# Optimization experiments

Hardware: AMD Instinct MI355X
Metric: run time of the kernel (lower is better)

The kernel has to match this reference:

```python
import jax, jax.numpy as jnp
import numpy as np

NSAMPLE = 1024
KNN = [16, 32, 64]
MLP = [[32, 32, 64], [64, 64, 128], [64, 96, 128]]
IN_CH = 3
EPS = 1e-5  # torch BatchNorm2d default eps


def fps(points, nsample):
    """Farthest point sampling. Deterministic start at index 0 (torch version uses a
    random start index; the algorithm/math is otherwise identical)."""
    B, N, _ = points.shape
    xyz = points[..., :3]

    def body(i, st):
        dist, far, idx = st
        idx = idx.at[:, i].set(far)
        c = jnp.take_along_axis(xyz, far[:, None, None], axis=1)  # [B,1,3]
        d = jnp.sum((xyz - c) ** 2, axis=-1)                      # [B,N]
        dist = jnp.minimum(dist, d)
        far = jnp.argmax(dist, axis=1).astype(jnp.int32)
        return dist, far, idx

    dist0 = jnp.full((B, N), 1e10, points.dtype)
    far0 = jnp.zeros((B,), jnp.int32)
    idx0 = jnp.zeros((B, nsample), jnp.int32)
    _, _, idx = jax.lax.fori_loop(0, nsample, body, (dist0, far0, idx0))
    return jnp.take_along_axis(points, idx[..., None], axis=1)  # [B,nsample,C]


def knn_idx(points, query, k):
    # Squared euclidean distances preserve the knn ordering of torch.cdist(p=2).
    q = query[..., :3]
    p = points[..., :3]
    d2 = (jnp.sum(q * q, -1)[:, :, None]
          - 2.0 * jnp.einsum('bqc,bnc->bqn', q, p)
          + jnp.sum(p * p, -1)[:, None, :])          # [B,S,N]
    return jax.lax.top_k(-d2, k)[1]                  # [B,S,k] smallest-k indices


def gather_groups(points, idx):
    return jax.vmap(lambda p, ix: p[ix])(points, idx)  # [B,S,k,C]


def mlp_branch(x, params):
    # x: [B,S,K,Cin]; 1x1 Conv2d == per-point linear; BN in training mode (batch stats).
    for w, b, g, be in params:
        x = jnp.einsum('bskc,oc->bsko', x, w) + b
        m = jnp.mean(x, axis=(0, 1, 2))
        v = jnp.var(x, axis=(0, 1, 2))
        x = jax.nn.relu((x - m) * jax.lax.rsqrt(v + EPS) * g + be)
    return jnp.max(x, axis=2)  # max-pool over neighbors -> [B,S,Cout]


def setup_inputs() -> dict:
    key = jax.random.key(0)
    ks = jax.random.split(key, 16)
    inp = {"points": jax.random.normal(ks[0], (8, 8192, 3), jnp.float32)}
    t = 1
    for i, block in enumerate(MLP):
        last = IN_CH
        for j, out in enumerate(block):
            inp[f"w{i}{j}"] = 0.1 * jax.random.normal(ks[t % 16], (out, last), jnp.float32)
            inp[f"b{i}{j}"] = jnp.zeros((out,), jnp.float32)
            inp[f"g{i}{j}"] = jnp.ones((out,), jnp.float32)
            inp[f"be{i}{j}"] = jnp.zeros((out,), jnp.float32)
            last = out
            t += 1
    return inp


def reference(points,
              w00, b00, g00, be00, w01, b01, g01, be01, w02, b02, g02, be02,
              w10, b10, g10, be10, w11, b11, g11, be11, w12, b12, g12, be12,
              w20, b20, g20, be20, w21, b21, g21, be21, w22, b22, g22, be22):
    params = [
        [(w00, b00, g00, be00), (w01, b01, g01, be01), (w02, b02, g02, be02)],
        [(w10, b10, g10, be10), (w11, b11, g11, be11), (w12, b12, g12, be12)],
        [(w20, b20, g20, be20), (w21, b21, g21, be21), (w22, b22, g22, be22)],
    ]
    # FPS is deterministic here, so the per-branch recomputation in the torch code
    # yields identical centroids; compute once.
    centroids = fps(points, NSAMPLE)
    feats = []
    for i, k in enumerate(KNN):
        idx = knn_idx(points, centroids, k)
        grouped = gather_groups(points, idx)
        feats.append(mlp_branch(grouped, params[i]))
    return jnp.concatenate(feats, axis=-1)  # [B, nsample, 320]
```

## Files before the change

kernel.cpp:

```cpp
#include <hip/hip_runtime.h>
#include <hip/hip_fp16.h>

#define DEVFN __device__ __forceinline__

typedef _Float16 v2h __attribute__((ext_vector_type(2)));

DEVFN float fdot2(v2h a, v2h b, float c) {
#if __has_builtin(__builtin_amdgcn_fdot2)
  return __builtin_amdgcn_fdot2(a, b, c, false);
#else
  return c + (float)a[0] * (float)b[0] + (float)a[1] * (float)b[1];
#endif
}

struct OpSum { DEVFN float operator()(float a, float b) const { return a + b; } };

template<int CH, int D, typename OP, int NV>
DEVFN void halve(float (&v)[NV], int lane, int& base) {
  if constexpr (D >= 1) {
    OP op;
    if constexpr (CH > 1) {
      constexpr int H = CH / 2;
      #pragma unroll
      for (int i = 0; i < H; ++i) {
        float send = (lane & D) ? v[i] : v[H + i];
        float r = __shfl_xor(send, D);
        float keep = (lane & D) ? v[H + i] : v[i];
        v[i] = op(keep, r);
      }
      if (lane & D) base += H;
      halve<H, (D >> 1), OP, NV>(v, lane, base);
    } else {
      v[0] = op(v[0], __shfl_xor(v[0], D));
      halve<CH, (D >> 1), OP, NV>(v, lane, base);
    }
  }
}

template<int CC, int NA, int T>
DEVFN void do_stats_w(const float (&a)[NA], float m, int tid, float* spart,
                      float* prow, int statoff) {
  float v[2 * CC];
  #pragma unroll
  for (int j = 0; j < CC; ++j) { float x = a[j]; v[2 * j] = m * x; v[2 * j + 1] = m * x * x; }
  int lane = tid & 63, base = 0;
  halve<2 * CC, 32, OpSum, 2 * CC>(v, lane, base);
  int wv = tid >> 6;
  spart[wv * 256 + base] = v[0];
  __syncthreads();
  constexpr int NW = T / 64;
  if (tid < 2 * CC) {
    float s2 = 0.f;
    #pragma unroll
    for (int w = 0; w < NW; ++w) s2 += spart[w * 256 + tid];
    prow[statoff + tid] = s2;
  }
  __syncthreads();
}

__global__ __launch_bounds__(512) void fps_kernel(const float* __restrict__ pts,
                                                  float4* __restrict__ cent) {
  const int b = blockIdx.x, t = threadIdx.x;
  const int wv = t >> 6;
  __shared__ unsigned long long sk2[2][8];
  __shared__ float4 sc4[2][8];
  __shared__ float4 scent[1024];
  const float* p = pts + (size_t)b * 8192 * 3;
  float px[16], py[16], pz[16], dd[16];
  #pragma unroll
  for (int j = 0; j < 16; ++j) {
    const int i = t + j * 512;
    px[j] = p[i * 3]; py[j] = p[i * 3 + 1]; pz[j] = p[i * 3 + 2];
    dd[j] = 1e10f;
  }
  float cx = p[0], cy = p[1], cz = p[2];
  for (int it = 0; it < 1024; ++it) {
    if (t == 0) scent[it] = make_float4(cx, cy, cz, 0.f);
    const int par = it & 1;
    float bd = -1.f, bx = 0.f, by = 0.f, bz = 0.f; int bi = 0;
    #pragma unroll
    for (int j = 0; j < 16; ++j) {
      const float dx = px[j] - cx, dy = py[j] - cy, dz = pz[j] - cz;
      float d = fminf(dd[j], dx * dx + dy * dy + dz * dz);
      dd[j] = d;
      if (d > bd) { bd = d; bi = t + j * 512; bx = px[j]; by = py[j]; bz = pz[j]; }
    }
    float wmax = bd;
    #pragma unroll
    for (int m = 32; m >= 1; m >>= 1) wmax = fmaxf(wmax, __shfl_xor(wmax, m));
    const unsigned long long am = __ballot(bd == wmax);
    bool iswin;
    if (__popcll(am) == 1) {
      iswin = (bd == wmax);
    } else {
      int cand = (bd == wmax) ? bi : 0x7FFFFFFF;
      #pragma unroll
      for (int m = 32; m >= 1; m >>= 1) cand = min(cand, __shfl_xor(cand, m));
      iswin = (bd == wmax) && (bi == cand);
    }
    if (iswin) {
      sk2[par][wv] = ((unsigned long long)__float_as_uint(bd) << 32)
                     | (0xFFFFFFFFu - (unsigned)bi);
      sc4[par][wv] = make_float4(bx, by, bz, 0.f);
    }
    __syncthreads();
    unsigned long long gk = sk2[par][0];
    float4 c4 = sc4[par][0];
    #pragma unroll
    for (int w = 1; w < 8; ++w) {
      const unsigned long long k2 = sk2[par][w];
      const float4 cc = sc4[par][w];
      if (k2 > gk) { gk = k2; c4 = cc; }
    }
    cx = c4.x; cy = c4.y; cz = c4.z;
  }
  __syncthreads();
  #pragma unroll
  for (int i = t; i < 1024; i += 512) cent[(size_t)b * 1024 + i] = scent[i];
}

__global__ __launch_bounds__(256) void knn_kernel(const float* __restrict__ pts,
                                                  const float4* __restrict__ cent,
                                                  int* __restrict__ knn) {
  const int wid = (blockIdx.x * 256 + threadIdx.x) >> 6;
  const int lane = threadIdx.x & 63;
  const int b = wid >> 10;
  const float4 q = cent[wid];
  const float q2 = q.x * q.x + q.y * q.y + q.z * q.z;
  const float* p = pts + (size_t)b * 8192 * 3;
  unsigned long long R = ~0ull;
  for (int c0 = 0; c0 < 8192; c0 += 64) {
    const int i = c0 + lane;
    const float x = p[i * 3], y = p[i * 3 + 1], z = p[i * 3 + 2];
    const float p2 = x * x + y * y + z * z;
    const float dot = q.x * x + q.y * y + q.z * z;
    float d2 = q2 - 2.f * dot + p2;
    d2 = fmaxf(d2, 0.f);
    unsigned u = __float_as_uint(d2);
    u = (u & 0x80000000u) ? ~u : (u | 0x80000000u);
    const unsigned long long key = ((unsigned long long)u << 32) | (unsigned)i;
    const unsigned long long rmax = __shfl(R, 63);
    unsigned long long mask = __ballot(key < rmax);
    while (mask) {
      const int src = __ffsll(mask) - 1;
      mask &= mask - 1;
      const unsigned long long nk = __shfl(key, src);
      const int pos = __popcll(__ballot(R < nk));
      if (pos < 64) {
        const unsigned long long Rm1 = __shfl_up(R, 1);
        R = (lane < pos) ? R : (lane == pos ? nk : Rm1);
      }
    }
  }
  knn[wid * 64 + lane] = (int)(R & 0xffffffffu);
}

__global__ __launch_bounds__(256) void moments_kernel(const float* __restrict__ pts,
                                                      const int* __restrict__ knn_,
                                                      float* __restrict__ mpart) {
  __shared__ float smom[4][27];
  const int tid = threadIdx.x, lane = tid & 63, wv = tid >> 6;
  const int samp = blockIdx.x * 4 + wv;
  const int b = samp >> 10;
  const int pidx = knn_[samp * 64 + lane];
  const float* pp = pts + ((size_t)b * 8192 + pidx) * 3;
  const float x = pp[0], y = pp[1], z = pp[2];
  float g[9] = {x, y, z, x * x, x * y, x * z, y * y, y * z, z * z};
  #pragma unroll
  for (int m = 8; m >= 1; m >>= 1) {
    #pragma unroll
    for (int i = 0; i < 9; ++i) g[i] += __shfl_xor(g[i], m);
  }
  float h[9], tot[9];
  #pragma unroll
  for (int i = 0; i < 9; ++i) h[i] = g[i] + __shfl_xor(g[i], 16);
  #pragma unroll
  for (int i = 0; i < 9; ++i) tot[i] = h[i] + __shfl_xor(h[i], 32);
  if (lane == 0) {
    #pragma unroll
    for (int i = 0; i < 9; ++i) {
      smom[wv][i] = g[i]; smom[wv][9 + i] = h[i]; smom[wv][18 + i] = tot[i];
    }
  }
  __syncthreads();
  if (tid < 27) {
    mpart[blockIdx.x * 32 + tid] =
        smom[0][tid] + smom[1][tid] + smom[2][tid] + smom[3][tid];
  }
}

__global__ __launch_bounds__(256) void finalize0_kernel(const float* __restrict__ mpart,
    const float* __restrict__ w00, const float* __restrict__ b00,
    const float* __restrict__ g00, const float* __restrict__ be00,
    const float* __restrict__ w01, const float* __restrict__ b01,
    const float* __restrict__ g01, const float* __restrict__ be01,
    const float* __restrict__ w02, const float* __restrict__ b02,
    const float* __restrict__ g02, const float* __restrict__ be02,
    float* __restrict__ scsh) {
  __shared__ float fsum[8][32];
  __shared__ float mom[32];
  const int t = threadIdx.x;
  const int col = t & 31, chunk = t >> 5;
  float s = 0.f;
  for (int r = chunk * 256; r < chunk * 256 + 256; ++r) s += mpart[r * 32 + col];
  fsum[chunk][col] = s;
  __syncthreads();
  if (t < 32) {
    float s2 = 0.f;
    #pragma unroll
    for (int c = 0; c < 8; ++c) s2 += fsum[c][t];
    mom[t] = s2;
  }
  __syncthreads();
  int o; const float *w, *bb, *gg, *be; float E; int base, br;
  if (t < 32)       { br = 0; o = t;      w = w00; bb = b00; gg = g00; be = be00; E = 131072.f; base = 0; }
  else if (t < 96)  { br = 1; o = t - 32; w = w01; bb = b01; gg = g01; be = be01; E = 262144.f; base = 9; }
  else if (t < 160) { br = 2; o = t - 96; w = w02; bb = b02; gg = g02; be = be02; E = 524288.f; base = 18; }
  else return;
  const float Sx = mom[base], Sy = mom[base + 1], Sz = mom[base + 2];
  const float mxx = mom[base + 3], mxy = mom[base + 4], mxz = mom[base + 5];
  const float myy = mom[base + 6], myz = mom[base + 7], mzz = mom[base + 8];
  const float W0 = w[o * 3], W1 = w[o * 3 + 1], W2 = w[o * 3 + 2], bo = bb[o];
  const float wS = W0 * Sx + W1 * Sy + W2 * Sz;
  const float qf = W0 * W0 * mxx + 2.f * W0 * W1 * mxy + 2.f * W0 * W2 * mxz
                 + W1 * W1 * myy + 2.f * W1 * W2 * myz + W2 * W2 * mzz;
  const float mean = wS / E + bo;
  const float msq = (qf + 2.f * bo * wS) / E + bo * bo;
  const float var = msq - mean * mean;
  const float inv = 1.0f / sqrtf(var + 1e-5f);
  const float sc = gg[o] * inv;
  scsh[br * 768 + o] = sc;
  scsh[br * 768 + 128 + o] = be[o] - mean * sc;
}

__global__ __launch_bounds__(256) void pack_kernel(
    const float* __restrict__ w1a, const float* __restrict__ w1b, const float* __restrict__ w1c,
    const float* __restrict__ w2a, const float* __restrict__ w2b, const float* __restrict__ w2c,
    v2h* __restrict__ w1h2, v2h* __restrict__ w2h2) {
  const int i = blockIdx.x * 256 + threadIdx.x;
  if (i < 512) {
    const int o = i >> 4, c2 = i & 15;
    w1h2[i] = v2h{(_Float16)w1a[o * 32 + 2 * c2], (_Float16)w1a[o * 32 + 2 * c2 + 1]};
  } else if (i < 2560) {
    const int j = i - 512, o = j >> 5, c2 = j & 31;
    w1h2[i] = v2h{(_Float16)w1b[o * 64 + 2 * c2], (_Float16)w1b[o * 64 + 2 * c2 + 1]};
  } else if (i < 5632) {
    const int j = i - 2560, o = j >> 5, c2 = j & 31;
    w1h2[i] = v2h{(_Float16)w1c[o * 64 + 2 * c2], (_Float16)w1c[o * 64 + 2 * c2 + 1]};
  } else if (i < 6656) {
    const int j = i - 5632, c2 = j >> 6, jj = j & 63;
    w2h2[j] = v2h{(_Float16)w2a[jj * 32 + 2 * c2], (_Float16)w2a[jj * 32 + 2 * c2 + 1]};
  } else if (i < 10752) {
    const int j = i - 6656, c2 = j >> 7, jj = j & 127;
    w2h2[1024 + j] = v2h{(_Float16)w2b[jj * 64 + 2 * c2], (_Float16)w2b[jj * 64 + 2 * c2 + 1]};
  } else if (i < 16896) {
    const int j = i - 10752, c2 = j >> 7, jj = j & 127;
    w2h2[5120 + j] = v2h{(_Float16)w2c[jj * 96 + 2 * c2], (_Float16)w2c[jj * 96 + 2 * c2 + 1]};
  }
}

__global__ __launch_bounds__(256) void zero_kernel(int* __restrict__ p, int n) {
  const int i = blockIdx.x * 256 + threadIdx.x;
  if (i < n) p[i] = 0;
}

__global__ __launch_bounds__(256) void hist_kernel(const int* __restrict__ knn_,
                                                   int* __restrict__ cnt) {
  const int e = blockIdx.x * 256 + threadIdx.x;
  const int s = e >> 6, k = e & 63;
  const int b = s >> 10;
  const int idx = b * 8192 + knn_[e];
  atomicAdd(&cnt[131072 + idx], 1);
  if (k < 32) atomicAdd(&cnt[65536 + idx], 1);
  if (k < 16) atomicAdd(&cnt[idx], 1);
}

__global__ __launch_bounds__(256) void reduce_rows_kernel(const float* __restrict__ partials,
                                                          int nb, float* __restrict__ out32) {
  const int r0 = blockIdx.x, j = threadIdx.x;
  const int chunk = (nb + 31) / 32;
  const int lo = r0 * chunk;
  const int hi = (lo + chunk < nb) ? lo + chunk : nb;
  float s = 0.f;
  for (int r = lo; r < hi; ++r) s += partials[(size_t)r * 256 + j];
  out32[r0 * 256 + j] = s;
}

__global__ __launch_bounds__(256) void finalize_kernel(const float* __restrict__ partials, int nb,
    const float* __restrict__ g, const float* __restrict__ be, float n,
    float* __restrict__ sc, float* __restrict__ sh, int CO) {
  __shared__ float tot[256];
  const int j = threadIdx.x;
  if (j < 2 * CO) {
    float s = 0.f;
    for (int r = 0; r < nb; ++r) s += partials[(size_t)r * 256 + j];
    tot[j] = s;
  }
  __syncthreads();
  if (j < CO) {
    const float m = tot[2 * j] / n;
    const float v = tot[2 * j + 1] / n - m * m;
    const float inv = 1.0f / sqrtf(v + 1e-5f);
    const float scv = g[j] * inv;
    sc[j] = scv;
    sh[j] = be[j] - m * scv;
  }
}

template<int C0, int C1, int T>
__global__ __launch_bounds__(T) void pass1_kernel(
    const float* __restrict__ pts, const int* __restrict__ cnt,
    const float* __restrict__ w0, const float* __restrict__ b0,
    const v2h* __restrict__ w1p, const float* __restrict__ b1,
    const float* __restrict__ scshb, float* __restrict__ partials,
    __half* __restrict__ x1pts) {
  constexpr int C02 = C0 / 2;
  __shared__ float spart[(T / 64) * 256];
  const int tid = threadIdx.x;
  const int pt = blockIdx.x * T + tid;
  const float m = (float)cnt[pt];
  const float* pp = pts + (size_t)pt * 3;
  float* prow = partials + (size_t)blockIdx.x * 256;
  const float zx = pp[0], zy = pp[1], zz = pp[2];
  const float* sc0 = scshb;
  const float* sh0 = scshb + 128;
  v2h a0p[C02];
  #pragma unroll
  for (int c2 = 0; c2 < C02; ++c2) {
    float va = b0[2 * c2]     + zx * w0[6 * c2]     + zy * w0[6 * c2 + 1] + zz * w0[6 * c2 + 2];
    float vb = b0[2 * c2 + 1] + zx * w0[6 * c2 + 3] + zy * w0[6 * c2 + 4] + zz * w0[6 * c2 + 5];
    va = fmaxf(0.f, va * sc0[2 * c2] + sh0[2 * c2]);
    vb = fmaxf(0.f, vb * sc0[2 * c2 + 1] + sh0[2 * c2 + 1]);
    a0p[c2] = v2h{(_Float16)va, (_Float16)vb};
  }
  for (int CB = 0; CB < C1; CB += 32) {
    float arr[32];
    #pragma unroll
    for (int oo = 0; oo < 32; ++oo) {
      const int o = CB + oo;
      float s0 = 0.f, s1 = 0.f;
      #pragma unroll
      for (int c2 = 0; c2 < C02; c2 += 2) {
        s0 = fdot2(a0p[c2],     w1p[o * C02 + c2],     s0);
        s1 = fdot2(a0p[c2 + 1], w1p[o * C02 + c2 + 1], s1);
      }
      const float x = b1[o] + (s0 + s1);
      x1pts[(size_t)o * 65536 + pt] = __float2half(x);
      arr[oo] = x;
    }
    do_stats_w<32, 32, T>(arr, m, tid, spart, prow, 2 * CB);
  }
}

template<int C1, int C2, int T>
__global__ __launch_bounds__(T) void pass2_kernel(
    const __half* __restrict__ x1pts, const int* __restrict__ cnt,
    const v2h* __restrict__ w2p, const float* __restrict__ b2,
    const float* __restrict__ scshb, float* __restrict__ partials,
    float* __restrict__ x2pts) {
  constexpr int C12 = C1 / 2;
  constexpr int RSv = C12 + 1;
  __shared__ v2h arowv[T * RSv];
  __shared__ float spart[(T / 64) * 256];
  const int tid = threadIdx.x;
  const int pt = blockIdx.x * T + tid;
  const float m = (float)cnt[pt];
  float* prow = partials + (size_t)blockIdx.x * 256;
  const float* sc1 = scshb + 256;
  const float* sh1 = scshb + 384;
  for (int o2 = 0; o2 < C12; ++o2) {
    float xa = __half2float(x1pts[(size_t)(2 * o2) * 65536 + pt]);
    float xb = __half2float(x1pts[(size_t)(2 * o2 + 1) * 65536 + pt]);
    xa = fmaxf(0.f, xa * sc1[2 * o2] + sh1[2 * o2]);
    xb = fmaxf(0.f, xb * sc1[2 * o2 + 1] + sh1[2 * o2 + 1]);
    arowv[tid * RSv + o2] = v2h{(_Float16)xa, (_Float16)xb};
  }
  for (int CB = 0; CB < C2; CB += 32) {
    float acc[32];
    #pragma unroll
    for (int j = 0; j < 32; ++j) acc[j] = b2[CB + j];
    for (int c2 = 0; c2 < C12; ++c2) {
      const v2h az = arowv[tid * RSv + c2];
      const v2h* wrow = w2p + c2 * C2 + CB;
      #pragma unroll
      for (int j = 0; j < 32; ++j) acc[j] = fdot2(az, wrow[j], acc[j]);
    }
    #pragma unroll
    for (int j = 0; j < 32; ++j) x2pts[(size_t)pt * C2 + CB + j] = acc[j];
    do_stats_w<32, 32, T>(acc, m, tid, spart, prow, 2 * CB);
  }
}

template<int K_, int C2, int BOFF>
__global__ __launch_bounds__(C2) void pool_kernel(const float* __restrict__ x2pts,
                                                  const int* __restrict__ knn_,
                                                  const float* __restrict__ scshb,
                                                  float* __restrict__ out) {
  const int s = blockIdx.x;
  const int c = threadIdx.x;
  const int b = s >> 10;
  const float sc = scshb[512 + c], sh = scshb[640 + c];
  const int* kn = knn_ + s * 64;
  float mx = -1e30f, mn = 1e30f;
  for (int k = 0; k < K_; ++k) {
    const int idx = kn[k];
    const float x = x2pts[((size_t)(b * 8192 + idx)) * C2 + c];
    mx = fmaxf(mx, x); mn = fminf(mn, x);
  }
  const float xv = (sc >= 0.f) ? mx : mn;
  out[(size_t)s * 320 + BOFF + c] = fmaxf(0.f, fmaf(sc, xv, sh));
}

template<int K_, int C0, int C1, int C2, int BOFF>
static void run_branch(const float* pts, const int* knn_, const int* cntb,
                       const float* const* W_, const float* const* B_,
                       const float* const* G_, const float* const* BE_,
                       float* scshb, float* partials, float* partials2,
                       const v2h* w1pb, const v2h* w2pb,
                       __half* x1pts, float* x2pts, float* out, hipStream_t stream) {
  constexpr int T = 128;
  constexpr int NB = 65536 / T;
  const float NEf = (float)(8 * 1024 * K_);
  pass1_kernel<C0, C1, T><<<NB, T, 0, stream>>>(
      pts, cntb, W_[0], B_[0], w1pb, B_[1], scshb, partials, x1pts);
  reduce_rows_kernel<<<32, 256, 0, stream>>>(partials, NB, partials2);
  finalize_kernel<<<1, 256, 0, stream>>>(partials2, 32, G_[1], BE_[1], NEf,
                                         scshb + 256, scshb + 384, C1);
  pass2_kernel<C1, C2, T><<<NB, T, 0, stream>>>(
      x1pts, cntb, w2pb, B_[2], scshb, partials, x2pts);
  reduce_rows_kernel<<<32, 256, 0, stream>>>(partials, NB, partials2);
  finalize_kernel<<<1, 256, 0, stream>>>(partials2, 32, G_[2], BE_[2], NEf,
                                         scshb + 512, scshb + 640, C2);
  pool_kernel<K_, C2, BOFF><<<8192, C2, 0, stream>>>(x2pts, knn_, scshb, out);
}

extern "C" void kernel_launch(void* const* d_in, const int* in_sizes, int n_in,
                              void* d_out, int out_size, void* d_ws, size_t ws_size,
                              hipStream_t stream) {
  (void)in_sizes; (void)n_in; (void)out_size; (void)ws_size;
  const float* pts = (const float*)d_in[0];
  const float* W_[9]; const float* B_[9]; const float* G_[9]; const float* BE_[9];
  for (int m = 0; m < 9; ++m) {
    W_[m]  = (const float*)d_in[1 + m * 4 + 0];
    B_[m]  = (const float*)d_in[1 + m * 4 + 1];
    G_[m]  = (const float*)d_in[1 + m * 4 + 2];
    BE_[m] = (const float*)d_in[1 + m * 4 + 3];
  }
  char* ws = (char*)d_ws;
  float4* cent      = (float4*)ws;
  int*    knn_      = (int*)(ws + 131072);
  float*  partials  = (float*)(ws + 2228224);
  float*  scsh      = (float*)(ws + 6422528);
  v2h*    w1h2      = (v2h*)(ws + 6434816);
  v2h*    w2h2      = (v2h*)(ws + 6457344);
  float*  partials2 = (float*)(ws + 6502400);
  int*    cnt       = (int*)(ws + 6535168);
  __half* x1pts     = (__half*)(ws + 7321600);
  float*  x2pts     = (float*)(ws + 19904512);
  float*  out       = (float*)d_out;

  fps_kernel<<<8, 512, 0, stream>>>(pts, cent);
  knn_kernel<<<2048, 256, 0, stream>>>(pts, cent, knn_);
  moments_kernel<<<2048, 256, 0, stream>>>(pts, knn_, partials);
  finalize0_kernel<<<1, 256, 0, stream>>>(partials,
      W_[0], B_[0], G_[0], BE_[0], W_[3], B_[3], G_[3], BE_[3],
      W_[6], B_[6], G_[6], BE_[6], scsh);
  pack_kernel<<<66, 256, 0, stream>>>(W_[1], W_[4], W_[7], W_[2], W_[5], W_[8], w1h2, w2h2);
  zero_kernel<<<768, 256, 0, stream>>>(cnt, 196608);
  hist_kernel<<<2048, 256, 0, stream>>>(knn_, cnt);

  run_branch<16, 32, 32, 64, 0>(pts, knn_, cnt, W_ + 0, B_ + 0, G_ + 0, BE_ + 0,
      scsh, partials, partials2, w1h2, w2h2, x1pts, x2pts, out, stream);
  run_branch<32, 64, 64, 128, 64>(pts, knn_, cnt + 65536, W_ + 3, B_ + 3, G_ + 3, BE_ + 3,
      scsh + 768, partials, partials2, w1h2 + 512, w2h2 + 1024, x1pts, x2pts, out, stream);
  run_branch<64, 64, 96, 128, 192>(pts, knn_, cnt + 131072, W_ + 6, B_ + 6, G_ + 6, BE_ + 6,
      scsh + 1536, partials, partials2, w1h2 + 2560, w2h2 + 5120, x1pts, x2pts, out, stream);
}
```

Measured before the change: 1.887 ms.

## Fuse knn with histogram and moments, store activations as half2, drop reduce step

Merges the histogram and first-layer moment computation into the knn kernel, so the separate moments and hist kernels and the reload of knn indices go away. Intermediate activations x1 and x2 are now stored as packed half2 (x2 was fp32), which halves the traffic in pass2 and pool. The pool kernel now handles channel pairs with 256-thread blocks. The reduce_rows stage is removed, so finalize sums all 512 partial rows in a single block. The risks are lower precision in the x2 max-pool and a serial reduction inside finalize.

```diff
diff --git a/kernel.cpp b/kernel.cpp
--- a/kernel.cpp
+++ b/kernel.cpp
@@ -121,9 +121,14 @@
 
 __global__ __launch_bounds__(256) void knn_kernel(const float* __restrict__ pts,
                                                   const float4* __restrict__ cent,
-                                                  int* __restrict__ knn) {
-  const int wid = (blockIdx.x * 256 + threadIdx.x) >> 6;
-  const int lane = threadIdx.x & 63;
+                                                  int* __restrict__ knn,
+                                                  int* __restrict__ cnt,
+                                                  float* __restrict__ mpart) {
+  __shared__ float smom[4][27];
+  const int tid = threadIdx.x;
+  const int wv = tid >> 6;
+  const int wid = blockIdx.x * 4 + wv;
+  const int lane = tid & 63;
   const int b = wid >> 10;
   const float4 q = cent[wid];
   const float q2 = q.x * q.x + q.y * q.y + q.z * q.z;
@@ -152,18 +157,15 @@
       }
     }
   }
-  knn[wid * 64 + lane] = (int)(R & 0xffffffffu);
-}
-
-__global__ __launch_bounds__(256) void moments_kernel(const float* __restrict__ pts,
-                                                      const int* __restrict__ knn_,
-                                                      float* __restrict__ mpart) {
-  __shared__ float smom[4][27];
-  const int tid = threadIdx.x, lane = tid & 63, wv = tid >> 6;
-  const int samp = blockIdx.x * 4 + wv;
-  const int b = samp >> 10;
-  const int pidx = knn_[samp * 64 + lane];
-  const float* pp = pts + ((size_t)b * 8192 + pidx) * 3;
+  const int nidx = (int)(R & 0xffffffffu);
+  knn[wid * 64 + lane] = nidx;
+
+  const int gidx = b * 8192 + nidx;
+  atomicAdd(&cnt[131072 + gidx], 1);
+  if (lane < 32) atomicAdd(&cnt[65536 + gidx], 1);
+  if (lane < 16) atomicAdd(&cnt[gidx], 1);
+
+  const float* pp = pts + (size_t)gidx * 3;
   const float x = pp[0], y = pp[1], z = pp[2];
   float g[9] = {x, y, z, x * x, x * y, x * z, y * y, y * z, z * z};
   #pragma unroll
@@ -264,28 +266,6 @@
   if (i < n) p[i] = 0;
 }
 
-__global__ __launch_bounds__(256) void hist_kernel(const int* __restrict__ knn_,
-                                                   int* __restrict__ cnt) {
-  const int e = blockIdx.x * 256 + threadIdx.x;
-  const int s = e >> 6, k = e & 63;
-  const int b = s >> 10;
-  const int idx = b * 8192 + knn_[e];
-  atomicAdd(&cnt[131072 + idx], 1);
-  if (k < 32) atomicAdd(&cnt[65536 + idx], 1);
-  if (k < 16) atomicAdd(&cnt[idx], 1);
-}
-
-__global__ __launch_bounds__(256) void reduce_rows_kernel(const float* __restrict__ partials,
-                                                          int nb, float* __restrict__ out32) {
-  const int r0 = blockIdx.x, j = threadIdx.x;
-  const int chunk = (nb + 31) / 32;
-  const int lo = r0 * chunk;
-  const int hi = (lo + chunk < nb) ? lo + chunk : nb;
-  float s = 0.f;
-  for (int r = lo; r < hi; ++r) s += partials[(size_t)r * 256 + j];
-  out32[r0 * 256 + j] = s;
-}
-
 __global__ __launch_bounds__(256) void finalize_kernel(const float* __restrict__ partials, int nb,
     const float* __restrict__ g, const float* __restrict__ be, float n,
     float* __restrict__ sc, float* __restrict__ sh, int CO) {
@@ -313,7 +293,7 @@
     const float* __restrict__ w0, const float* __restrict__ b0,
     const v2h* __restrict__ w1p, const float* __restrict__ b1,
     const float* __restrict__ scshb, float* __restrict__ partials,
-    __half* __restrict__ x1pts) {
+    __half2* __restrict__ x1h2) {
   constexpr int C02 = C0 / 2;
   __shared__ float spart[(T / 64) * 256];
   const int tid = threadIdx.x;
@@ -344,21 +324,23 @@
         s0 = fdot2(a0p[c2],     w1p[o * C02 + c2],     s0);
         s1 = fdot2(a0p[c2 + 1], w1p[o * C02 + c2 + 1], s1);
       }
-      const float x = b1[o] + (s0 + s1);
-      x1pts[(size_t)o * 65536 + pt] = __float2half(x);
-      arr[oo] = x;
-    }
+      arr[oo] = b1[o] + (s0 + s1);
+    }
+    #pragma unroll
+    for (int j = 0; j < 16; ++j)
+      x1h2[(size_t)(CB / 2 + j) * 65536 + pt] = __floats2half2_rn(arr[2 * j], arr[2 * j + 1]);
     do_stats_w<32, 32, T>(arr, m, tid, spart, prow, 2 * CB);
   }
 }
 
 template<int C1, int C2, int T>
 __global__ __launch_bounds__(T) void pass2_kernel(
-    const __half* __restrict__ x1pts, const int* __restrict__ cnt,
+    const __half2* __restrict__ x1h2, const int* __restrict__ cnt,
     const v2h* __restrict__ w2p, const float* __restrict__ b2,
     const float* __restrict__ scshb, float* __restrict__ partials,
-    float* __restrict__ x2pts) {
+    __half2* __restrict__ x2h2) {
   constexpr int C12 = C1 / 2;
+  constexpr int CP = C2 / 2;
   constexpr int RSv = C12 + 1;
   __shared__ v2h arowv[T * RSv];
   __shared__ float spart[(T / 64) * 256];
@@ -369,10 +351,9 @@
   const float* sc1 = scshb + 256;
   const float* sh1 = scshb + 384;
   for (int o2 = 0; o2 < C12; ++o2) {
-    float xa = __half2float(x1pts[(size_t)(2 * o2) * 65536 + pt]);
-    float xb = __half2float(x1pts[(size_t)(2 * o2 + 1) * 65536 + pt]);
-    xa = fmaxf(0.f, xa * sc1[2 * o2] + sh1[2 * o2]);
-    xb = fmaxf(0.f, xb * sc1[2 * o2 + 1] + sh1[2 * o2 + 1]);
+    const float2 f = __half22float2(x1h2[(size_t)o2 * 65536 + pt]);
+    const float xa = fmaxf(0.f, f.x * sc1[2 * o2] + sh1[2 * o2]);
+    const float xb = fmaxf(0.f, f.y * sc1[2 * o2 + 1] + sh1[2 * o2 + 1]);
     arowv[tid * RSv + o2] = v2h{(_Float16)xa, (_Float16)xb};
   }
   for (int CB = 0; CB < C2; CB += 32) {
@@ -386,52 +367,58 @@
       for (int j = 0; j < 32; ++j) acc[j] = fdot2(az, wrow[j], acc[j]);
     }
     #pragma unroll
-    for (int j = 0; j < 32; ++j) x2pts[(size_t)pt * C2 + CB + j] = acc[j];
+    for (int j = 0; j < 16; ++j)
+      x2h2[(size_t)pt * CP + CB / 2 + j] = __floats2half2_rn(acc[2 * j], acc[2 * j + 1]);
     do_stats_w<32, 32, T>(acc, m, tid, spart, prow, 2 * CB);
   }
 }
 
 template<int K_, int C2, int BOFF>
-__global__ __launch_bounds__(C2) void pool_kernel(const float* __restrict__ x2pts,
-                                                  const int* __restrict__ knn_,
-                                                  const float* __restrict__ scshb,
-                                                  float* __restrict__ out) {
-  const int s = blockIdx.x;
-  const int c = threadIdx.x;
+__global__ __launch_bounds__(256) void pool_kernel(const __half2* __restrict__ x2h2,
+                                                   const int* __restrict__ knn_,
+                                                   const float* __restrict__ scshb,
+                                                   float* __restrict__ out) {
+  constexpr int CP = C2 / 2;
+  const int g = blockIdx.x * 256 + threadIdx.x;
+  const int cp = g % CP;
+  const int s = g / CP;
   const int b = s >> 10;
-  const float sc = scshb[512 + c], sh = scshb[640 + c];
   const int* kn = knn_ + s * 64;
-  float mx = -1e30f, mn = 1e30f;
+  float mx0 = -1e30f, mx1 = -1e30f, mn0 = 1e30f, mn1 = 1e30f;
   for (int k = 0; k < K_; ++k) {
     const int idx = kn[k];
-    const float x = x2pts[((size_t)(b * 8192 + idx)) * C2 + c];
-    mx = fmaxf(mx, x); mn = fminf(mn, x);
-  }
-  const float xv = (sc >= 0.f) ? mx : mn;
-  out[(size_t)s * 320 + BOFF + c] = fmaxf(0.f, fmaf(sc, xv, sh));
+    const float2 f = __half22float2(x2h2[(size_t)(b * 8192 + idx) * CP + cp]);
+    mx0 = fmaxf(mx0, f.x); mn0 = fminf(mn0, f.x);
+    mx1 = fmaxf(mx1, f.y); mn1 = fminf(mn1, f.y);
+  }
+  const float sca = scshb[512 + 2 * cp], scb = scshb[512 + 2 * cp + 1];
+  const float sha = scshb[640 + 2 * cp], shb = scshb[640 + 2 * cp + 1];
+  float2 r;
+  r.x = fmaxf(0.f, fmaf(sca, (sca >= 0.f) ? mx0 : mn0, sha));
+  r.y = fmaxf(0.f, fmaf(scb, (scb >= 0.f) ? mx1 : mn1, shb));
+  *(float2*)&out[(size_t)s * 320 + BOFF + 2 * cp] = r;
 }
 
 template<int K_, int C0, int C1, int C2, int BOFF>
 static void run_branch(const float* pts, const int* knn_, const int* cntb,
                        const float* const* W_, const float* const* B_,
                        const float* const* G_, const float* const* BE_,
-                       float* scshb, float* partials, float* partials2,
+                       float* scshb, float* partials,
                        const v2h* w1pb, const v2h* w2pb,
-                       __half* x1pts, float* x2pts, float* out, hipStream_t stream) {
+                       __half2* x1h2, __half2* x2h2, float* out, hipStream_t stream) {
   constexpr int T = 128;
   constexpr int NB = 65536 / T;
   const float NEf = (float)(8 * 1024 * K_);
   pass1_kernel<C0, C1, T><<<NB, T, 0, stream>>>(
-      pts, cntb, W_[0], B_[0], w1pb, B_[1], scshb, partials, x1pts);
-  reduce_rows_kernel<<<32, 256, 0, stream>>>(partials, NB, partials2);
-  finalize_kernel<<<1, 256, 0, stream>>>(partials2, 32, G_[1], BE_[1], NEf,
+      pts, cntb, W_[0], B_[0], w1pb, B_[1], scshb, partials, x1h2);
+  finalize_kernel<<<1, 256, 0, stream>>>(partials, NB, G_[1], BE_[1], NEf,
                                          scshb + 256, scshb + 384, C1);
   pass2_kernel<C1, C2, T><<<NB, T, 0, stream>>>(
-      x1pts, cntb, w2pb, B_[2], scshb, partials, x2pts);
-  reduce_rows_kernel<<<32, 256, 0, stream>>>(partials, NB, partials2);
-  finalize_kernel<<<1, 256, 0, stream>>>(partials2, 32, G_[2], BE_[2], NEf,
+      x1h2, cntb, w2pb, B_[2], scshb, partials, x2h2);
+  finalize_kernel<<<1, 256, 0, stream>>>(partials, NB, G_[2], BE_[2], NEf,
                                          scshb + 512, scshb + 640, C2);
-  pool_kernel<K_, C2, BOFF><<<8192, C2, 0, stream>>>(x2pts, knn_, scshb, out);
+  pool_kernel<K_, C2, BOFF><<<8192 * (C2 / 2) / 256, 256, 0, stream>>>(
+      x2h2, knn_, scshb, out);
 }
 
 extern "C" void kernel_launch(void* const* d_in, const int* in_sizes, int n_in,
@@ -447,32 +434,29 @@
     BE_[m] = (const float*)d_in[1 + m * 4 + 3];
   }
   char* ws = (char*)d_ws;
-  float4* cent      = (float4*)ws;
-  int*    knn_      = (int*)(ws + 131072);
-  float*  partials  = (float*)(ws + 2228224);
-  float*  scsh      = (float*)(ws + 6422528);
-  v2h*    w1h2      = (v2h*)(ws + 6434816);
-  v2h*    w2h2      = (v2h*)(ws + 6457344);
-  float*  partials2 = (float*)(ws + 6502400);
-  int*    cnt       = (int*)(ws + 6535168);
-  __half* x1pts     = (__half*)(ws + 7321600);
-  float*  x2pts     = (float*)(ws + 19904512);
-  float*  out       = (float*)d_out;
-
+  float4*  cent     = (float4*)ws;
+  int*     knn_     = (int*)(ws + 131072);
+  float*   partials = (float*)(ws + 2228224);
+  float*   scsh     = (float*)(ws + 6422528);
+  v2h*     w1h2     = (v2h*)(ws + 6434816);
+  v2h*     w2h2     = (v2h*)(ws + 6457344);
+  int*     cnt      = (int*)(ws + 6535168);
+  __half2* x1h2     = (__half2*)(ws + 7321600);
+  __half2* x2h2     = (__half2*)(ws + 19904512);
+  float*   out      = (float*)d_out;
+
+  zero_kernel<<<768, 256, 0, stream>>>(cnt, 196608);
   fps_kernel<<<8, 512, 0, stream>>>(pts, cent);
-  knn_kernel<<<2048, 256, 0, stream>>>(pts, cent, knn_);
-  moments_kernel<<<2048, 256, 0, stream>>>(pts, knn_, partials);
+  knn_kernel<<<2048, 256, 0, stream>>>(pts, cent, knn_, cnt, partials);
   finalize0_kernel<<<1, 256, 0, stream>>>(partials,
       W_[0], B_[0], G_[0], BE_[0], W_[3], B_[3], G_[3], BE_[3],
       W_[6], B_[6], G_[6], BE_[6], scsh);
   pack_kernel<<<66, 256, 0, stream>>>(W_[1], W_[4], W_[7], W_[2], W_[5], W_[8], w1h2, w2h2);
-  zero_kernel<<<768, 256, 0, stream>>>(cnt, 196608);
-  hist_kernel<<<2048, 256, 0, stream>>>(knn_, cnt);
 
   run_branch<16, 32, 32, 64, 0>(pts, knn_, cnt, W_ + 0, B_ + 0, G_ + 0, BE_ + 0,
-      scsh, partials, partials2, w1h2, w2h2, x1pts, x2pts, out, stream);
+      scsh, partials, w1h2, w2h2, x1h2, x2h2, out, stream);
   run_branch<32, 64, 64, 128, 64>(pts, knn_, cnt + 65536, W_ + 3, B_ + 3, G_ + 3, BE_ + 3,
-      scsh + 768, partials, partials2, w1h2 + 512, w2h2 + 1024, x1pts, x2pts, out, stream);
+      scsh + 768, partials, w1h2 + 512, w2h2 + 1024, x1h2, x2h2, out, stream);
   run_branch<64, 64, 96, 128, 192>(pts, knn_, cnt + 131072, W_ + 6, B_ + 6, G_ + 6, BE_ + 6,
-      scsh + 1536, partials, partials2, w1h2 + 2560, w2h2 + 5120, x1pts, x2pts, out, stream);
-}
+      scsh + 1536, partials, w1h2 + 2560, w2h2 + 5120, x1h2, x2h2, out, stream);
+}
```

Result: slower. 2.439 ms (+29.2%).
